# Performance work log

Measured on AMD Instinct MI355X. Metric: run time of the kernel, lower is better.

Reference implementation:

```python
import jax, jax.numpy as jnp
import numpy as np

N, E = 100000, 1600000
IN, EDGE_DIM, HID, OUT, HEADS = 128, 16, 32, 32, 2


def _glorot(key, shape, scale=0.1):
    return jax.random.normal(key, shape, dtype=jnp.float32) * scale


def setup_inputs() -> dict:
    key = jax.random.key(0)
    ks = jax.random.split(key, 20)
    HC1 = HEADS * HID
    return {
        "x": jax.random.normal(ks[0], (N, IN), dtype=jnp.float32),
        "edge_index": jax.random.randint(ks[1], (2, E), 0, N, dtype=jnp.int32),
        "edge_attr": jax.random.normal(ks[2], (E, EDGE_DIM), dtype=jnp.float32),
        # layer 1 (heads=HEADS, concat=True)
        "W1l": _glorot(ks[3], (IN, HC1)), "b1l": jnp.zeros((HC1,), jnp.float32),
        "W1r": _glorot(ks[4], (IN, HC1)), "b1r": jnp.zeros((HC1,), jnp.float32),
        "W1e": _glorot(ks[5], (EDGE_DIM, HC1)),
        "att1": _glorot(ks[6], (HEADS, HID)),
        "bias1": jnp.zeros((HC1,), jnp.float32),
        # layer 2 (heads=1, concat=False)
        "W2l": _glorot(ks[7], (HC1, HID)), "b2l": jnp.zeros((HID,), jnp.float32),
        "W2r": _glorot(ks[8], (HC1, HID)), "b2r": jnp.zeros((HID,), jnp.float32),
        "W2e": _glorot(ks[9], (EDGE_DIM, HID)),
        "att2": _glorot(ks[10], (1, HID)),
        "bias2": jnp.zeros((HID,), jnp.float32),
        # final linear
        "Wlin": _glorot(ks[11], (HID, OUT)), "blin": jnp.zeros((OUT,), jnp.float32),
    }


def gatv2_layer(x, src, dst, edge_attr, Wl, bl, Wr, br, We, att, bias, H, C, concat):
    n = x.shape[0]
    xl = (x @ Wl + bl).reshape(n, H, C)   # source transform (lin_l)
    xr = (x @ Wr + br).reshape(n, H, C)   # target transform (lin_r)
    ea = (edge_attr @ We).reshape(-1, H, C)
    m = xl[src] + xr[dst] + ea                       # [E, H, C]
    e = jnp.sum(jax.nn.leaky_relu(m, 0.2) * att, axis=-1)  # [E, H]
    # segment softmax over incoming edges of each destination node
    emax = jax.ops.segment_max(e, dst, num_segments=n)
    emax = jnp.where(jnp.isfinite(emax), emax, 0.0)
    ee = jnp.exp(e - emax[dst])
    denom = jax.ops.segment_sum(ee, dst, num_segments=n)
    alpha = ee / (denom[dst] + 1e-16)                # [E, H]
    out = jax.ops.segment_sum(xl[src] * alpha[..., None], dst, num_segments=n)  # [N, H, C]
    out = out.reshape(n, H * C) if concat else out.mean(axis=1)
    return out + bias


def reference(x, edge_index, edge_attr, W1l, b1l, W1r, b1r, W1e, att1, bias1,
              W2l, b2l, W2r, b2r, W2e, att2, bias2, Wlin, blin):
    src, dst = edge_index[0], edge_index[1]
    h = jax.nn.elu(gatv2_layer(x, src, dst, edge_attr, W1l, b1l, W1r, b1r, W1e,
                               att1, bias1, HEADS, HID, True))
    h = jax.nn.elu(gatv2_layer(h, src, dst, edge_attr, W2l, b2l, W2r, b2r, W2e,
                               att2, bias2, 1, HID, False))
    return h @ Wlin + blin
```

## Files before the change

kernel.cpp:

```cpp
#include <hip/hip_runtime.h>
#include <hip/hip_fp16.h>
#include <cstdint>
#include <cstddef>


typedef _Float16 half8 __attribute__((ext_vector_type(8)));
typedef float f32x4 __attribute__((ext_vector_type(4)));

__global__ void hist_kernel(const int* __restrict__ dst, int* __restrict__ deg, int E) {
    int e = blockIdx.x * blockDim.x + threadIdx.x;
    if (e < E) atomicAdd(&deg[dst[e]], 1);
}

__global__ void scan_part(const int* __restrict__ deg, int* __restrict__ bsum, int n) {
    int tid = threadIdx.x;
    int base = blockIdx.x * 1024 + tid * 4;
    int s = 0;
#pragma unroll
    for (int j = 0; j < 4; ++j) {
        int i = base + j;
        if (i < n) s += deg[i];
    }
#pragma unroll
    for (int off = 1; off < 64; off <<= 1) s += __shfl_xor(s, off, 64);
    __shared__ int ws[4];
    if ((tid & 63) == 0) ws[tid >> 6] = s;
    __syncthreads();
    if (tid == 0) bsum[blockIdx.x] = ws[0] + ws[1] + ws[2] + ws[3];
}

__global__ void scan_mid(int* __restrict__ bsum, int* __restrict__ rowstart, int nb, int n) {
    int tid = threadIdx.x;
    int v = (tid < nb) ? bsum[tid] : 0;
    int incl = v;
#pragma unroll
    for (int off = 1; off < 64; off <<= 1) {
        int t = __shfl_up(incl, off, 64);
        if ((tid & 63) >= off) incl += t;
    }
    __shared__ int w0;
    if (tid == 63) w0 = incl;
    __syncthreads();
    if (tid >= 64) incl += w0;
    if (tid < nb) bsum[tid] = incl - v;
    if (tid == nb - 1) rowstart[n] = incl;
}

__global__ void scan_fin(const int* __restrict__ deg, const int* __restrict__ bsum,
                         int* __restrict__ rowstart, int n) {
    int tid = threadIdx.x;
    int lane = tid & 63, wid = tid >> 6;
    int base = blockIdx.x * 1024 + tid * 4;
    int v[4];
    int s = 0;
#pragma unroll
    for (int j = 0; j < 4; ++j) {
        int i = base + j;
        v[j] = (i < n) ? deg[i] : 0;
        s += v[j];
    }
    int incl = s;
#pragma unroll
    for (int off = 1; off < 64; off <<= 1) {
        int t = __shfl_up(incl, off, 64);
        if (lane >= off) incl += t;
    }
    __shared__ int ws[4];
    if (lane == 63) ws[wid] = incl;
    __syncthreads();
    int wofs = 0;
    for (int w2 = 0; w2 < wid; ++w2) wofs += ws[w2];
    int acc = bsum[blockIdx.x] + wofs + (incl - s);
#pragma unroll
    for (int j = 0; j < 4; ++j) {
        int i = base + j;
        if (i < n) rowstart[i] = acc;
        acc += v[j];
    }
}

template <int K, int Mh>
__device__ void wprep_body(int i, const float* __restrict__ Wl, const float* __restrict__ Wr,
                           __half* __restrict__ Wfrag) {
    constexpr int KS = K / 32;
    if (i >= K * 2 * Mh) return;
    int j = i & 7;
    int lane = (i >> 3) & 63;
    int rest = i >> 9;
    int ks = rest % KS;
    int nt = rest / KS;
    int k = ks * 32 + ((lane >> 4) & 3) * 8 + j;
    int col = nt * 16 + (lane & 15);
    float v = (col < Mh) ? Wl[k * Mh + col] : Wr[k * Mh + (col - Mh)];
    Wfrag[i] = __float2half(v);
}

__global__ void wprep_both(const float* W1l, const float* W1r, __half* Wf1,
                           const float* W2l, const float* W2r, __half* Wf2) {
    int bid = blockIdx.x;
    int tid = threadIdx.x;
    if (bid < 64) wprep_body<128, 64>(bid * 256 + tid, W1l, W1r, Wf1);
    else          wprep_body<64, 32>((bid - 64) * 256 + tid, W2l, W2r, Wf2);
}

template <int K, int Mh, int BM>
__device__ void gemm_body(int bid, __half* xs, const float* __restrict__ x,
                          const __half* __restrict__ Wfrag, const float* __restrict__ bl,
                          const float* __restrict__ br, __half* __restrict__ yl,
                          __half* __restrict__ yr, int n) {
    constexpr int KS = K / 32;
    constexpr int NT = (2 * Mh) / 16;
    constexpr int RW = BM / 64;
    constexpr int LDP = K + 8;
    int tid = threadIdx.x;
    int lane = tid & 63;
    int wave = tid >> 6;
    int node0 = bid * BM;
    constexpr int ITER = (BM * K) / (256 * 4);
#pragma unroll
    for (int it = 0; it < ITER; ++it) {
        int base = (it * 256 + tid) * 4;
        int row = base / K, kk = base % K;
        float4 v = make_float4(0.f, 0.f, 0.f, 0.f);
        if (node0 + row < n) v = *(const float4*)&x[(size_t)(node0 + row) * K + kk];
        __half2* d = (__half2*)&xs[row * LDP + kk];
        d[0] = __float22half2_rn(make_float2(v.x, v.y));
        d[1] = __float22half2_rn(make_float2(v.z, v.w));
    }
    __syncthreads();
    f32x4 acc[RW][NT];
#pragma unroll
    for (int r = 0; r < RW; ++r)
#pragma unroll
        for (int t = 0; t < NT; ++t) {
            f32x4 z = {0.f, 0.f, 0.f, 0.f};
            acc[r][t] = z;
        }
    int r0 = lane & 15, kof = (lane >> 4) * 8;
#pragma unroll
    for (int ks = 0; ks < KS; ++ks) {
        half8 a[RW];
#pragma unroll
        for (int r = 0; r < RW; ++r) {
            int row = (wave * RW + r) * 16 + r0;
            a[r] = *reinterpret_cast<const half8*>(&xs[row * LDP + ks * 32 + kof]);
        }
#pragma unroll
        for (int t = 0; t < NT; ++t) {
            half8 b = *reinterpret_cast<const half8*>(&Wfrag[(((size_t)t * KS + ks) * 64 + lane) * 8]);
#pragma unroll
            for (int r = 0; r < RW; ++r)
                acc[r][t] = __builtin_amdgcn_mfma_f32_16x16x32_f16(a[r], b, acc[r][t], 0, 0, 0);
        }
    }
#pragma unroll
    for (int r = 0; r < RW; ++r) {
#pragma unroll
        for (int t = 0; t < NT; ++t) {
            int col = t * 16 + (lane & 15);
            float bv = (col < Mh) ? bl[col] : br[col - Mh];
#pragma unroll
            for (int q = 0; q < 4; ++q) {
                int node = node0 + (wave * RW + r) * 16 + (lane >> 4) * 4 + q;
                if (node < n) {
                    float v = acc[r][t][q] + bv;
                    if (col < Mh) yl[(size_t)node * Mh + col] = __float2half(v);
                    else          yr[(size_t)node * Mh + (col - Mh)] = __float2half(v);
                }
            }
        }
    }
}

__device__ void scatter_body(int e, const int* __restrict__ src, const int* __restrict__ dst,
                             const float* __restrict__ eattr, const int* __restrict__ rowstart,
                             int* __restrict__ cursor, int2* __restrict__ es,
                             __half* __restrict__ eah, int E) {
    if (e < E) {
        int d = dst[e];
        int p = atomicAdd(&cursor[d], 1);
        es[rowstart[d] + p] = make_int2(e, src[e]);
        const float4* s4 = (const float4*)&eattr[(size_t)e * 16];
        float4 a = s4[0], b = s4[1], c = s4[2], f = s4[3];
        __half2 h[8];
        h[0] = __float22half2_rn(make_float2(a.x, a.y));
        h[1] = __float22half2_rn(make_float2(a.z, a.w));
        h[2] = __float22half2_rn(make_float2(b.x, b.y));
        h[3] = __float22half2_rn(make_float2(b.z, b.w));
        h[4] = __float22half2_rn(make_float2(c.x, c.y));
        h[5] = __float22half2_rn(make_float2(c.z, c.w));
        h[6] = __float22half2_rn(make_float2(f.x, f.y));
        h[7] = __float22half2_rn(make_float2(f.z, f.w));
        int4* o = (int4*)&eah[(size_t)e * 16];
        o[0] = *(int4*)&h[0];
        o[1] = *(int4*)&h[4];
    }
}

__device__ void dcount_body(int bid, int* h, const int* __restrict__ deg,
                            int* __restrict__ counts, int n) {
    int tid = threadIdx.x;
    h[tid] = 0;
    __syncthreads();
    int base = bid * 4096;
#pragma unroll
    for (int j = 0; j < 16; ++j) {
        int i = base + j * 256 + tid;
        if (i < n) {
            int b = deg[i];
            b = (b > 255) ? 255 : b;
            atomicAdd(&h[b], 1);
        }
    }
    __syncthreads();
    counts[bid * 256 + tid] = h[tid];
}

__global__ __launch_bounds__(256) void fat_kernel(
    int nbG, int nbS,
    const float* __restrict__ x, const __half* __restrict__ Wf1,
    const float* __restrict__ b1l, const float* __restrict__ b1r,
    __half* __restrict__ A, __half* __restrict__ B, int n,
    const int* __restrict__ src, const int* __restrict__ dst,
    const float* __restrict__ eattr, const int* __restrict__ rowstart,
    int* __restrict__ cursor, int2* __restrict__ es, __half* __restrict__ eah, int E,
    const int* __restrict__ deg, int* __restrict__ counts) {
    __shared__ __half xs[64 * 136];
    __shared__ int hcnt[256];
    int bid = blockIdx.x;
    if (bid < nbG) {
        gemm_body<128, 64, 64>(bid, xs, x, Wf1, b1l, b1r, A, B, n);
    } else if (bid < nbG + nbS) {
        scatter_body((bid - nbG) * 256 + threadIdx.x, src, dst, eattr, rowstart, cursor, es,
                     eah, E);
    } else {
        dcount_body(bid - nbG - nbS, hcnt, deg, counts, n);
    }
}

__global__ void dbase_kernel(const int* __restrict__ counts, int* __restrict__ base, int nblk) {
    int b = threadIdx.x;
    int tot = 0;
    for (int k = 0; k < nblk; ++k) tot += counts[k * 256 + b];
    __shared__ int ws[4];
    int lane = b & 63, wid = b >> 6;
    int incl = tot;
#pragma unroll
    for (int off = 1; off < 64; off <<= 1) {
        int t = __shfl_up(incl, off, 64);
        if (lane >= off) incl += t;
    }
    if (lane == 63) ws[wid] = incl;
    __syncthreads();
    int wofs = 0;
    for (int w = 0; w < wid; ++w) wofs += ws[w];
    int acc = wofs + incl - tot;
    for (int k = 0; k < nblk; ++k) {
        base[k * 256 + b] = acc;
        acc += counts[k * 256 + b];
    }
}

__global__ __launch_bounds__(256) void dscatter_block(const int* __restrict__ deg,
                                                      const int* __restrict__ base,
                                                      int* __restrict__ nodeperm, int n) {
    __shared__ int h[256];
    int tid = threadIdx.x;
    h[tid] = 0;
    __syncthreads();
    int bbase = blockIdx.x * 4096;
#pragma unroll
    for (int j = 0; j < 16; ++j) {
        int i = bbase + j * 256 + tid;
        if (i < n) {
            int b = deg[i];
            b = (b > 255) ? 255 : b;
            int r = atomicAdd(&h[b], 1);
            nodeperm[base[blockIdx.x * 256 + b] + r] = i;
        }
    }
}

template <int K, int Mh, int BM>
__global__ __launch_bounds__(256) void gemm_mfma(
    const float* __restrict__ x, const __half* __restrict__ Wfrag,
    const float* __restrict__ bl, const float* __restrict__ br,
    __half* __restrict__ yl, __half* __restrict__ yr, int n) {
    __shared__ __half xs[BM * (K + 8)];
    gemm_body<K, Mh, BM>(blockIdx.x, xs, x, Wfrag, bl, br, yl, yr, n);
}

template <int K, int M, int NPB>
__global__ void linear_kernel(const float* __restrict__ x, const float* __restrict__ W,
                              const float* __restrict__ b, float* __restrict__ y, int n) {
    __shared__ float sx[NPB * K];
    int tid = threadIdx.x;
    int node0 = blockIdx.x * NPB;
    for (int i = tid; i < NPB * K; i += NPB * M) {
        int nn = node0 + i / K;
        sx[i] = (nn < n) ? x[(size_t)nn * K + (i % K)] : 0.f;
    }
    __syncthreads();
    int ln = tid / M, m = tid % M;
    int node = node0 + ln;
    if (node >= n) return;
    float acc = b[m];
#pragma unroll
    for (int k = 0; k < K; ++k) acc = fmaf(sx[ln * K + k], W[k * M + m], acc);
    y[(size_t)node * M + m] = acc;
}

template <int H, int C>
__global__ __launch_bounds__(256) void fused_edge_agg(
    const int* __restrict__ rowstart, const int2* __restrict__ es,
    const __half* __restrict__ eah, const int* __restrict__ nodeperm,
    const float* __restrict__ We,
    const float* __restrict__ att,
    const __half* __restrict__ xl, const __half* __restrict__ xr,
    const float* __restrict__ bias, float* __restrict__ out, int n) {
    constexpr int HC = H * C;
    constexpr int LPN = HC / 2;
    constexpr int NPW = 64 / LPN;
    int gt = blockIdx.x * blockDim.x + threadIdx.x;
    int wave = gt >> 6;
    int lane = threadIdx.x & 63;
    int sub = lane / LPN;
    int j = lane % LPN;
    int ch0 = 2 * j;
    int slot = wave * NPW + sub;
    if (slot >= n) return;
    int node = nodeperm[slot];
    __half2 wh[16];
#pragma unroll
    for (int k = 0; k < 16; ++k) wh[k] = __float22half2_rn(*(const float2*)&We[k * HC + ch0]);
    float2 a2 = *(const float2*)&att[ch0];
    float2 xr2 = __half22float2(*(const __half2*)&xr[(size_t)node * HC + ch0]);
    int beg = rowstart[node], end = rowstart[node + 1];
    float denom = 0.f, acc0 = 0.f, acc1 = 0.f;

    auto gemv = [&](const float4& r0, const float4& r1, const __half2& xlh,
                    float& m0, float& m1, float2& xlf) {
        const __half2* h0 = (const __half2*)&r0;
        const __half2* h1 = (const __half2*)&r1;
        __half2 p0 = __hmul2(__low2half2(h0[0]), wh[0]);
        __half2 p1 = __hmul2(__high2half2(h0[0]), wh[1]);
        p0 = __hfma2(__low2half2(h0[1]), wh[2], p0);
        p1 = __hfma2(__high2half2(h0[1]), wh[3], p1);
        p0 = __hfma2(__low2half2(h0[2]), wh[4], p0);
        p1 = __hfma2(__high2half2(h0[2]), wh[5], p1);
        p0 = __hfma2(__low2half2(h0[3]), wh[6], p0);
        p1 = __hfma2(__high2half2(h0[3]), wh[7], p1);
        p0 = __hfma2(__low2half2(h1[0]), wh[8], p0);
        p1 = __hfma2(__high2half2(h1[0]), wh[9], p1);
        p0 = __hfma2(__low2half2(h1[1]), wh[10], p0);
        p1 = __hfma2(__high2half2(h1[1]), wh[11], p1);
        p0 = __hfma2(__low2half2(h1[2]), wh[12], p0);
        p1 = __hfma2(__high2half2(h1[2]), wh[13], p1);
        p0 = __hfma2(__low2half2(h1[3]), wh[14], p0);
        p1 = __hfma2(__high2half2(h1[3]), wh[15], p1);
        float2 mf = __half22float2(__hadd2(p0, p1));
        xlf = __half22float2(xlh);
        m0 = xlf.x + xr2.x + mf.x;
        m1 = xlf.y + xr2.y + mf.y;
    };
    auto logit = [&](float m0, float m1) -> float {
        m0 = (m0 > 0.f) ? m0 : 0.2f * m0;
        m1 = (m1 > 0.f) ? m1 : 0.2f * m1;
        float v = m0 * a2.x + m1 * a2.y;
#pragma unroll
        for (int msk = 1; msk < 16; msk <<= 1) v += __shfl_xor(v, msk, 64);
        return v;
    };

    int pp = beg;
    for (; pp + 2 <= end; pp += 2) {
        int2 ea = es[pp];
        int2 eb = es[pp + 1];
        const float4* qa = (const float4*)&eah[(size_t)ea.x * 16];
        const float4* qb = (const float4*)&eah[(size_t)eb.x * 16];
        float4 r0a = qa[0], r1a = qa[1];
        float4 r0b = qb[0], r1b = qb[1];
        __half2 xh0 = *(const __half2*)&xl[(size_t)ea.y * HC + ch0];
        __half2 xh1 = *(const __half2*)&xl[(size_t)eb.y * HC + ch0];
        float m0a, m1a, m0b, m1b;
        float2 xla, xlb;
        gemv(r0a, r1a, xh0, m0a, m1a, xla);
        gemv(r0b, r1b, xh1, m0b, m1b, xlb);
        float wa = __expf(logit(m0a, m1a));
        float wb = __expf(logit(m0b, m1b));
        denom += wa + wb;
        acc0 = fmaf(xla.x, wa, acc0);
        acc1 = fmaf(xla.y, wa, acc1);
        acc0 = fmaf(xlb.x, wb, acc0);
        acc1 = fmaf(xlb.y, wb, acc1);
    }
    if (pp < end) {
        int2 ea = es[pp];
        const float4* qa = (const float4*)&eah[(size_t)ea.x * 16];
        float4 r0a = qa[0], r1a = qa[1];
        __half2 xh0 = *(const __half2*)&xl[(size_t)ea.y * HC + ch0];
        float m0a, m1a;
        float2 xla;
        gemv(r0a, r1a, xh0, m0a, m1a, xla);
        float wa = __expf(logit(m0a, m1a));
        denom += wa;
        acc0 = fmaf(xla.x, wa, acc0);
        acc1 = fmaf(xla.y, wa, acc1);
    }
    float2 b2 = *(const float2*)&bias[ch0];
    float inv = 1.f / (denom + 1e-16f);
    float o0 = acc0 * inv + b2.x;
    float o1 = acc1 * inv + b2.y;
    o0 = (o0 > 0.f) ? o0 : __expf(o0) - 1.f;
    o1 = (o1 > 0.f) ? o1 : __expf(o1) - 1.f;
    *(float2*)&out[(size_t)node * HC + ch0] = make_float2(o0, o1);
}

extern "C" void kernel_launch(void* const* d_in, const int* in_sizes, int n_in,
                              void* d_out, int out_size, void* d_ws, size_t ws_size,
                              hipStream_t stream) {
    const float* x     = (const float*)d_in[0];
    const int*   eidx  = (const int*)d_in[1];
    const float* eattr = (const float*)d_in[2];
    const float* W1l   = (const float*)d_in[3];
    const float* b1l   = (const float*)d_in[4];
    const float* W1r   = (const float*)d_in[5];
    const float* b1r   = (const float*)d_in[6];
    const float* W1e   = (const float*)d_in[7];
    const float* att1  = (const float*)d_in[8];
    const float* bias1 = (const float*)d_in[9];
    const float* W2l   = (const float*)d_in[10];
    const float* b2l   = (const float*)d_in[11];
    const float* W2r   = (const float*)d_in[12];
    const float* b2r   = (const float*)d_in[13];
    const float* W2e   = (const float*)d_in[14];
    const float* att2  = (const float*)d_in[15];
    const float* bias2 = (const float*)d_in[16];
    const float* Wlin  = (const float*)d_in[17];
    const float* blin  = (const float*)d_in[18];

    const int N = in_sizes[0] / 128;
    const int E = in_sizes[1] / 2;
    const int* src = eidx;
    const int* dst = eidx + E;
    const int NB_DC = (N + 4095) / 4096;

    char* p = (char*)d_ws;
    auto take = [&](size_t bytes) {
        char* r = p;
        p += (bytes + 255) & ~(size_t)255;
        return r;
    };
    int*    deg      = (int*)take((size_t)N * sizeof(int));
    int*    cursor   = (int*)take((size_t)N * sizeof(int));
    char*   zero_end = p;
    int*    rowstart = (int*)take((size_t)(N + 1) * sizeof(int));
    int*    bsum     = (int*)take(256 * sizeof(int));
    int*    counts   = (int*)take((size_t)(NB_DC + 1) * 256 * sizeof(int));
    int*    dbase    = (int*)take((size_t)(NB_DC + 1) * 256 * sizeof(int));
    int*    nodeperm = (int*)take((size_t)N * sizeof(int));
    int2*   es       = (int2*)take((size_t)E * sizeof(int2));
    __half* eah      = (__half*)take((size_t)E * 16 * sizeof(__half));
    __half* A        = (__half*)take((size_t)N * 64 * sizeof(__half));
    __half* B        = (__half*)take((size_t)N * 64 * sizeof(__half));
    float*  Cbuf     = (float*)take((size_t)N * 64 * sizeof(float));
    __half* Wf1      = (__half*)take((size_t)128 * 128 * sizeof(__half));
    __half* Wf2      = (__half*)take((size_t)64 * 64 * sizeof(__half));

    (void)hipMemsetAsync(deg, 0, (size_t)(zero_end - (char*)deg), stream);
    hist_kernel<<<(E + 255) / 256, 256, 0, stream>>>(dst, deg, E);
    {
        int nb = (N + 1023) / 1024;
        scan_part<<<nb, 256, 0, stream>>>(deg, bsum, N);
        scan_mid<<<1, 128, 0, stream>>>(bsum, rowstart, nb, N);
        scan_fin<<<nb, 256, 0, stream>>>(deg, bsum, rowstart, N);
    }
    wprep_both<<<80, 256, 0, stream>>>(W1l, W1r, Wf1, W2l, W2r, Wf2);

    {
        int nbG = (N + 63) / 64;
        int nbS = (E + 255) / 256;
        fat_kernel<<<nbG + nbS + NB_DC, 256, 0, stream>>>(
            nbG, nbS, x, Wf1, b1l, b1r, A, B, N, src, dst, eattr, rowstart, cursor, es, eah, E,
            deg, counts);
    }
    dbase_kernel<<<1, 256, 0, stream>>>(counts, dbase, NB_DC);
    dscatter_block<<<NB_DC, 256, 0, stream>>>(deg, dbase, nodeperm, N);

    {
        long waves = (N + 1) / 2;
        fused_edge_agg<2, 32><<<(int)((waves * 64 + 255) / 256), 256, 0, stream>>>(
            rowstart, es, eah, nodeperm, W1e, att1, A, B, bias1, Cbuf, N);
    }

    gemm_mfma<64, 32, 128><<<(N + 127) / 128, 256, 0, stream>>>(Cbuf, Wf2, b2l, b2r, A, B, N);
    {
        long waves = (N + 3) / 4;
        fused_edge_agg<1, 32><<<(int)((waves * 64 + 255) / 256), 256, 0, stream>>>(
            rowstart, es, eah, nodeperm, W2e, att2, A, B, bias2, Cbuf, N);
    }

    linear_kernel<32, 32, 8><<<(N + 7) / 8, 256, 0, stream>>>(Cbuf, Wlin, blin, (float*)d_out, N);
}
```

Measured before the change: 408.0 us.

## Store intermediate node features in fp16 and fuse histogram with weight prep

Intermediate layer outputs move from an fp32 buffer to fp16. The edge-aggregation kernels write half2, and the second GEMM and the final linear read half. Histogram and weight-fragment prep are merged into one launch, and the fat kernel is reordered so scatter blocks come before GEMM blocks. The goal is to cut intermediate memory traffic and one launch, at the cost of extra fp16 rounding in the layer-1 and layer-2 outputs.

```diff
diff --git a/kernel.cpp b/kernel.cpp
--- a/kernel.cpp
+++ b/kernel.cpp
@@ -6,11 +6,6 @@
 
 typedef _Float16 half8 __attribute__((ext_vector_type(8)));
 typedef float f32x4 __attribute__((ext_vector_type(4)));
-
-__global__ void hist_kernel(const int* __restrict__ dst, int* __restrict__ deg, int E) {
-    int e = blockIdx.x * blockDim.x + threadIdx.x;
-    if (e < E) atomicAdd(&deg[dst[e]], 1);
-}
 
 __global__ void scan_part(const int* __restrict__ deg, int* __restrict__ bsum, int n) {
     int tid = threadIdx.x;
@@ -95,16 +90,23 @@
     Wfrag[i] = __float2half(v);
 }
 
-__global__ void wprep_both(const float* W1l, const float* W1r, __half* Wf1,
+__global__ void pre_kernel(int nbH, const int* __restrict__ dst, int* __restrict__ deg, int E,
+                           const float* W1l, const float* W1r, __half* Wf1,
                            const float* W2l, const float* W2r, __half* Wf2) {
     int bid = blockIdx.x;
     int tid = threadIdx.x;
-    if (bid < 64) wprep_body<128, 64>(bid * 256 + tid, W1l, W1r, Wf1);
-    else          wprep_body<64, 32>((bid - 64) * 256 + tid, W2l, W2r, Wf2);
-}
-
-template <int K, int Mh, int BM>
-__device__ void gemm_body(int bid, __half* xs, const float* __restrict__ x,
+    if (bid < nbH) {
+        int e = bid * 256 + tid;
+        if (e < E) atomicAdd(&deg[dst[e]], 1);
+    } else {
+        int wb = bid - nbH;
+        if (wb < 64) wprep_body<128, 64>(wb * 256 + tid, W1l, W1r, Wf1);
+        else         wprep_body<64, 32>((wb - 64) * 256 + tid, W2l, W2r, Wf2);
+    }
+}
+
+template <int K, int Mh, int BM, bool HALFIN>
+__device__ void gemm_body(int bid, __half* xs, const void* xin,
                           const __half* __restrict__ Wfrag, const float* __restrict__ bl,
                           const float* __restrict__ br, __half* __restrict__ yl,
                           __half* __restrict__ yr, int n) {
@@ -116,16 +118,30 @@
     int lane = tid & 63;
     int wave = tid >> 6;
     int node0 = bid * BM;
-    constexpr int ITER = (BM * K) / (256 * 4);
-#pragma unroll
-    for (int it = 0; it < ITER; ++it) {
-        int base = (it * 256 + tid) * 4;
-        int row = base / K, kk = base % K;
-        float4 v = make_float4(0.f, 0.f, 0.f, 0.f);
-        if (node0 + row < n) v = *(const float4*)&x[(size_t)(node0 + row) * K + kk];
-        __half2* d = (__half2*)&xs[row * LDP + kk];
-        d[0] = __float22half2_rn(make_float2(v.x, v.y));
-        d[1] = __float22half2_rn(make_float2(v.z, v.w));
+    if constexpr (!HALFIN) {
+        const float* x = (const float*)xin;
+        constexpr int ITER = (BM * K) / (256 * 4);
+#pragma unroll
+        for (int it = 0; it < ITER; ++it) {
+            int base = (it * 256 + tid) * 4;
+            int row = base / K, kk = base % K;
+            float4 v = make_float4(0.f, 0.f, 0.f, 0.f);
+            if (node0 + row < n) v = *(const float4*)&x[(size_t)(node0 + row) * K + kk];
+            __half2* d = (__half2*)&xs[row * LDP + kk];
+            d[0] = __float22half2_rn(make_float2(v.x, v.y));
+            d[1] = __float22half2_rn(make_float2(v.z, v.w));
+        }
+    } else {
+        const __half* x = (const __half*)xin;
+        constexpr int ITER = (BM * K) / (256 * 8);
+#pragma unroll
+        for (int it = 0; it < ITER; ++it) {
+            int base = (it * 256 + tid) * 8;
+            int row = base / K, kk = base % K;
+            int4 v = make_int4(0, 0, 0, 0);
+            if (node0 + row < n) v = *(const int4*)&x[(size_t)(node0 + row) * K + kk];
+            *(int4*)&xs[row * LDP + kk] = v;
+        }
     }
     __syncthreads();
     f32x4 acc[RW][NT];
@@ -217,7 +233,7 @@
 }
 
 __global__ __launch_bounds__(256) void fat_kernel(
-    int nbG, int nbS,
+    int nbS, int nbG,
     const float* __restrict__ x, const __half* __restrict__ Wf1,
     const float* __restrict__ b1l, const float* __restrict__ b1r,
     __half* __restrict__ A, __half* __restrict__ B, int n,
@@ -228,13 +244,12 @@
     __shared__ __half xs[64 * 136];
     __shared__ int hcnt[256];
     int bid = blockIdx.x;
-    if (bid < nbG) {
-        gemm_body<128, 64, 64>(bid, xs, x, Wf1, b1l, b1r, A, B, n);
-    } else if (bid < nbG + nbS) {
-        scatter_body((bid - nbG) * 256 + threadIdx.x, src, dst, eattr, rowstart, cursor, es,
-                     eah, E);
+    if (bid < nbS) {
+        scatter_body(bid * 256 + threadIdx.x, src, dst, eattr, rowstart, cursor, es, eah, E);
+    } else if (bid < nbS + nbG) {
+        gemm_body<128, 64, 64, false>(bid - nbS, xs, x, Wf1, b1l, b1r, A, B, n);
     } else {
-        dcount_body(bid - nbG - nbS, hcnt, deg, counts, n);
+        dcount_body(bid - nbS - nbG, hcnt, deg, counts, n);
     }
 }
 
@@ -282,23 +297,23 @@
 }
 
 template <int K, int Mh, int BM>
-__global__ __launch_bounds__(256) void gemm_mfma(
-    const float* __restrict__ x, const __half* __restrict__ Wfrag,
+__global__ __launch_bounds__(256) void gemm_mfma_h(
+    const __half* __restrict__ x, const __half* __restrict__ Wfrag,
     const float* __restrict__ bl, const float* __restrict__ br,
     __half* __restrict__ yl, __half* __restrict__ yr, int n) {
     __shared__ __half xs[BM * (K + 8)];
-    gemm_body<K, Mh, BM>(blockIdx.x, xs, x, Wfrag, bl, br, yl, yr, n);
+    gemm_body<K, Mh, BM, true>(blockIdx.x, xs, x, Wfrag, bl, br, yl, yr, n);
 }
 
 template <int K, int M, int NPB>
-__global__ void linear_kernel(const float* __restrict__ x, const float* __restrict__ W,
+__global__ void linear_kernel(const __half* __restrict__ x, const float* __restrict__ W,
                               const float* __restrict__ b, float* __restrict__ y, int n) {
     __shared__ float sx[NPB * K];
     int tid = threadIdx.x;
     int node0 = blockIdx.x * NPB;
     for (int i = tid; i < NPB * K; i += NPB * M) {
         int nn = node0 + i / K;
-        sx[i] = (nn < n) ? x[(size_t)nn * K + (i % K)] : 0.f;
+        sx[i] = (nn < n) ? __half2float(x[(size_t)nn * K + (i % K)]) : 0.f;
     }
     __syncthreads();
     int ln = tid / M, m = tid % M;
@@ -317,7 +332,7 @@
     const float* __restrict__ We,
     const float* __restrict__ att,
     const __half* __restrict__ xl, const __half* __restrict__ xr,
-    const float* __restrict__ bias, float* __restrict__ out, int n) {
+    const float* __restrict__ bias, __half* __restrict__ out, int n) {
     constexpr int HC = H * C;
     constexpr int LPN = HC / 2;
     constexpr int NPW = 64 / LPN;
@@ -413,7 +428,7 @@
     float o1 = acc1 * inv + b2.y;
     o0 = (o0 > 0.f) ? o0 : __expf(o0) - 1.f;
     o1 = (o1 > 0.f) ? o1 : __expf(o1) - 1.f;
-    *(float2*)&out[(size_t)node * HC + ch0] = make_float2(o0, o1);
+    *(__half2*)&out[(size_t)node * HC + ch0] = __float22half2_rn(make_float2(o0, o1));
 }
 
 extern "C" void kernel_launch(void* const* d_in, const int* in_sizes, int n_in,
@@ -463,25 +478,27 @@
     __half* eah      = (__half*)take((size_t)E * 16 * sizeof(__half));
     __half* A        = (__half*)take((size_t)N * 64 * sizeof(__half));
     __half* B        = (__half*)take((size_t)N * 64 * sizeof(__half));
-    float*  Cbuf     = (float*)take((size_t)N * 64 * sizeof(float));
+    __half* Chalf    = (__half*)take((size_t)N * 64 * sizeof(__half));
     __half* Wf1      = (__half*)take((size_t)128 * 128 * sizeof(__half));
     __half* Wf2      = (__half*)take((size_t)64 * 64 * sizeof(__half));
 
     (void)hipMemsetAsync(deg, 0, (size_t)(zero_end - (char*)deg), stream);
-    hist_kernel<<<(E + 255) / 256, 256, 0, stream>>>(dst, deg, E);
+    {
+        int nbH = (E + 255) / 256;
+        pre_kernel<<<nbH + 80, 256, 0, stream>>>(nbH, dst, deg, E, W1l, W1r, Wf1, W2l, W2r, Wf2);
+    }
     {
         int nb = (N + 1023) / 1024;
         scan_part<<<nb, 256, 0, stream>>>(deg, bsum, N);
         scan_mid<<<1, 128, 0, stream>>>(bsum, rowstart, nb, N);
         scan_fin<<<nb, 256, 0, stream>>>(deg, bsum, rowstart, N);
     }
-    wprep_both<<<80, 256, 0, stream>>>(W1l, W1r, Wf1, W2l, W2r, Wf2);
 
     {
+        int nbS = (E + 255) / 256;
         int nbG = (N + 63) / 64;
-        int nbS = (E + 255) / 256;
-        fat_kernel<<<nbG + nbS + NB_DC, 256, 0, stream>>>(
-            nbG, nbS, x, Wf1, b1l, b1r, A, B, N, src, dst, eattr, rowstart, cursor, es, eah, E,
+        fat_kernel<<<nbS + nbG + NB_DC, 256, 0, stream>>>(
+            nbS, nbG, x, Wf1, b1l, b1r, A, B, N, src, dst, eattr, rowstart, cursor, es, eah, E,
             deg, counts);
     }
     dbase_kernel<<<1, 256, 0, stream>>>(counts, dbase, NB_DC);
@@ -490,15 +507,15 @@
     {
         long waves = (N + 1) / 2;
         fused_edge_agg<2, 32><<<(int)((waves * 64 + 255) / 256), 256, 0, stream>>>(
-            rowstart, es, eah, nodeperm, W1e, att1, A, B, bias1, Cbuf, N);
-    }
-
-    gemm_mfma<64, 32, 128><<<(N + 127) / 128, 256, 0, stream>>>(Cbuf, Wf2, b2l, b2r, A, B, N);
+            rowstart, es, eah, nodeperm, W1e, att1, A, B, bias1, Chalf, N);
+    }
+
+    gemm_mfma_h<64, 32, 128><<<(N + 127) / 128, 256, 0, stream>>>(Chalf, Wf2, b2l, b2r, A, B, N);
     {
         long waves = (N + 3) / 4;
         fused_edge_agg<1, 32><<<(int)((waves * 64 + 255) / 256), 256, 0, stream>>>(
-            rowstart, es, eah, nodeperm, W2e, att2, A, B, bias2, Cbuf, N);
-    }
-
-    linear_kernel<32, 32, 8><<<(N + 7) / 8, 256, 0, stream>>>(Cbuf, Wlin, blin, (float*)d_out, N);
-}
+            rowstart, es, eah, nodeperm, W2e, att2, A, B, bias2, Chalf, N);
+    }
+
+    linear_kernel<32, 32, 8><<<(N + 7) / 8, 256, 0, stream>>>(Chalf, Wlin, blin, (float*)d_out, N);
+}
```

Result: slower. 419.9 us (+2.9%).
